# Kernel optimization log

Measured on AMD Instinct MI355X. Metric: run time of the kernel, lower is better.

## Reference

```python
import jax, jax.numpy as jnp
import numpy as np

B, T, IDIM = 16, 1024, 345
L, D, H, DK, FF = 4, 256, 4, 64, 1024
EPS = 1e-5


def layer_norm(x, s, b):
    m = jnp.mean(x, axis=-1, keepdims=True)
    v = jnp.mean(jnp.square(x - m), axis=-1, keepdims=True)
    return (x - m) * jax.lax.rsqrt(v + EPS) * s + b


def setup_inputs() -> dict:
    key = jax.random.key(0)
    ks = jax.random.split(key, 16)
    w = 0.02
    return {
        "x": jax.random.normal(ks[0], (B, T, IDIM), jnp.float32),
        "num_frames": int(T),
        "Win": w * jax.random.normal(ks[1], (IDIM, D), jnp.float32),
        "b_in": jnp.zeros((D,), jnp.float32),
        "ln1_s": jnp.ones((L, D), jnp.float32),
        "ln1_b": jnp.zeros((L, D), jnp.float32),
        "Wq": w * jax.random.normal(ks[2], (L, D, D), jnp.float32),
        "bq": jnp.zeros((L, D), jnp.float32),
        "Wk": w * jax.random.normal(ks[3], (L, D, D), jnp.float32),
        "bk": jnp.zeros((L, D), jnp.float32),
        "Wv": w * jax.random.normal(ks[4], (L, D, D), jnp.float32),
        "bv": jnp.zeros((L, D), jnp.float32),
        "Wo": w * jax.random.normal(ks[5], (L, D, D), jnp.float32),
        "bo": jnp.zeros((L, D), jnp.float32),
        "ln2_s": jnp.ones((L, D), jnp.float32),
        "ln2_b": jnp.zeros((L, D), jnp.float32),
        "W1": w * jax.random.normal(ks[6], (L, D, FF), jnp.float32),
        "b1": jnp.zeros((L, FF), jnp.float32),
        "W2": w * jax.random.normal(ks[7], (L, FF, D), jnp.float32),
        "b2": jnp.zeros((L, D), jnp.float32),
        "lno_s": jnp.ones((D,), jnp.float32),
        "lno_b": jnp.zeros((D,), jnp.float32),
    }


def reference(x, num_frames, Win, b_in, ln1_s, ln1_b, Wq, bq, Wk, bk, Wv, bv,
              Wo, bo, ln2_s, ln2_b, W1, b1, W2, b2, lno_s, lno_b):
    num = x.shape[0]
    scale = 1.0 / np.sqrt(DK)
    # [num*T, D]
    e = x.reshape(-1, x.shape[-1]) @ Win + b_in
    for i in range(L):
        e = layer_norm(e, ln1_s[i], ln1_b[i])
        # naive MHSA (residual taken from LN output, as in the source)
        q = (e @ Wq[i] + bq[i]).reshape(num, -1, H, DK)
        k = (e @ Wk[i] + bk[i]).reshape(num, -1, H, DK)
        v = (e @ Wv[i] + bv[i]).reshape(num, -1, H, DK)
        scores = jnp.einsum('bqhd,bkhd->bhqk', q, k) * scale
        attn = jax.nn.softmax(scores, axis=-1)
        o = jnp.einsum('bhqk,bkhd->bqhd', attn, v).reshape(-1, D)
        e = e + (o @ Wo[i] + bo[i])
        e = layer_norm(e, ln2_s[i], ln2_b[i])
        e = e + (jax.nn.relu(e @ W1[i] + b1[i]) @ W2[i] + b2[i])
    out = layer_norm(e, lno_s, lno_b)
    return out.reshape(num, num_frames, -1)
```

## Files before the change

kernel.cpp:

```cpp
#include <hip/hip_runtime.h>
#include <hip/hip_bf16.h>

#define BB    16
#define TT    1024
#define MTOK  (BB*TT)
#define IDIM_ 345
#define KPAD  384
#define LL    4
#define DD_   256
#define FF_   1024
#define EPS_  1e-5f
#define QSCL  0.18033688f
#define MSHIFT 12.0f

typedef __bf16 bf16;
typedef bf16 bf16x8 __attribute__((ext_vector_type(8)));
typedef float f32x4 __attribute__((ext_vector_type(4)));

static __device__ __forceinline__ f32x4 MFMA(bf16x8 a, bf16x8 b, f32x4 c) {
  return __builtin_amdgcn_mfma_f32_16x16x32_bf16(a, b, c, 0, 0, 0);
}
static __device__ __forceinline__ unsigned bfbits(float x) {
  return (unsigned)__builtin_bit_cast(unsigned short, (bf16)x);
}
static __device__ __forceinline__ bf16x8 ld_bf8(const void* p) {
  return *reinterpret_cast<const bf16x8*>(p);
}
static __device__ __forceinline__ void gload_lds16(const bf16* g, void* l) {
  __builtin_amdgcn_global_load_lds(
      (const __attribute__((address_space(1))) void*)g,
      (__attribute__((address_space(3))) void*)l, 16, 0, 0);
}

__global__ void k_convert_pad(const float* __restrict__ src, bf16* __restrict__ dst) {
  int idx = blockIdx.x * 256 + threadIdx.x;
  if (idx >= MTOK * (KPAD / 4)) return;
  int r = idx / (KPAD / 4), c0 = (idx % (KPAD / 4)) * 4;
  const float* s = src + (long)r * IDIM_ + c0;
  float v0 = (c0 + 0 < IDIM_) ? s[0] : 0.f;
  float v1 = (c0 + 1 < IDIM_) ? s[1] : 0.f;
  float v2 = (c0 + 2 < IDIM_) ? s[2] : 0.f;
  float v3 = (c0 + 3 < IDIM_) ? s[3] : 0.f;
  uint2 pk;
  pk.x = bfbits(v0) | (bfbits(v1) << 16);
  pk.y = bfbits(v2) | (bfbits(v3) << 16);
  *reinterpret_cast<uint2*>(dst + (long)r * KPAD + c0) = pk;
}

__global__ void k_wt_convert(const float* __restrict__ src, bf16* __restrict__ dst,
                             int K, int N, int Kp) {
  int idx = blockIdx.x * 256 + threadIdx.x;
  if (idx >= N * Kp) return;
  int n = idx / Kp, kk = idx % Kp;
  dst[idx] = (kk < K) ? (bf16)src[(long)kk * N + n] : (bf16)0.f;
}

__global__ __launch_bounds__(256)
void k_wt_all(const float* __restrict__ Wq, const float* __restrict__ Wk,
              const float* __restrict__ Wv, const float* __restrict__ Wo,
              const float* __restrict__ W1, const float* __restrict__ W2,
              bf16* __restrict__ Wqkvt, bf16* __restrict__ Wot,
              bf16* __restrict__ W1t, bf16* __restrict__ W2t) {
  __shared__ float tile[64][65];
  const int s = blockIdx.y, m = s >> 2, i = s & 3;
  const float* src; bf16* dst; int K, N;
  switch (m) {
    case 0: src = Wq + (long)i*65536;  dst = Wqkvt + (long)i*196608;          K=256;  N=256;  break;
    case 1: src = Wk + (long)i*65536;  dst = Wqkvt + (long)i*196608 + 65536;  K=256;  N=256;  break;
    case 2: src = Wv + (long)i*65536;  dst = Wqkvt + (long)i*196608 + 131072; K=256;  N=256;  break;
    case 3: src = Wo + (long)i*65536;  dst = Wot + (long)i*65536;             K=256;  N=256;  break;
    case 4: src = W1 + (long)i*262144; dst = W1t + (long)i*262144;            K=256;  N=1024; break;
    default:src = W2 + (long)i*262144; dst = W2t + (long)i*262144;            K=1024; N=256;  break;
  }
  const int tiles_n = N >> 6, ntiles = (K >> 6) * tiles_n;
  if (blockIdx.x >= ntiles) return;
  const int tk = blockIdx.x / tiles_n, tn = blockIdx.x % tiles_n;
  const int t = threadIdx.x, rq = t >> 6, cl = t & 63;
  #pragma unroll
  for (int i2 = 0; i2 < 16; i2++)
    tile[rq * 16 + i2][cl] = src[(long)(tk * 64 + rq * 16 + i2) * N + tn * 64 + cl];
  __syncthreads();
  #pragma unroll
  for (int i2 = 0; i2 < 16; i2++)
    dst[(long)(tn * 64 + rq * 16 + i2) * K + tk * 64 + cl] = (bf16)tile[cl][rq * 16 + i2];
}

__global__ void k_bias_concat(const float* __restrict__ bq, const float* __restrict__ bk,
                              const float* __restrict__ bv, float* __restrict__ bqkv) {
  int idx = blockIdx.x * 256 + threadIdx.x;
  if (idx >= LL * 768) return;
  int i = idx / 768, j = idx % 768;
  float v = (j < 256) ? bq[i*256 + j] : (j < 512 ? bk[i*256 + j - 256] : bv[i*256 + j - 512]);
  bqkv[idx] = v;
}

template<int EPI>
__global__ __launch_bounds__(512, 4)
void k_gemm_row(const bf16* __restrict__ A, const bf16* __restrict__ Wt,
                const float* __restrict__ bias, const bf16* __restrict__ resid,
                const float* __restrict__ lns, const float* __restrict__ lnb,
                void* __restrict__ out, int K) {
  __shared__ alignas(16) char As[4096];
  __shared__ alignas(16) char Bs[32768];
  __shared__ alignas(16) float redS[32][4];
  __shared__ alignas(16) float redQ[32][4];
  const int t = threadIdx.x, lane = t & 63, wid = t >> 6;
  const int wr = wid >> 2, wc = wid & 3;
  const int g = lane >> 4, c = lane & 15;
  int flat = blockIdx.x;
  flat = (flat & 7) * 64 + (flat >> 3);
  const int mbase = flat * 32;

  const int srow = t >> 3;
  const int slot = ((t & 7) ^ (srow & 7)) * 8;
  const bf16* ag = A  + (long)(mbase + srow) * K + slot;
  const bf16* bg = Wt + (long)srow * K + slot;
  const int swz = (c & 7) << 4;

  f32x4 acc[4] = {};

  const int nk = K >> 6;
  for (int kt = 0; kt < nk; ++kt) {
    const int k0 = kt * 64;
    __syncthreads();
    if (wid < 4) gload_lds16(ag + k0, As + wid * 1024);
    #pragma unroll
    for (int p = 0; p < 4; p++)
      gload_lds16(bg + (long)(p * 64) * K + k0, Bs + p * 8192 + wid * 1024);
    __syncthreads();

    bf16x8 af[2], bfr[4][2];
    #pragma unroll
    for (int ks = 0; ks < 2; ks++)
      af[ks] = ld_bf8(As + (wr * 16 + c) * 128 + ((ks * 64 + g * 16) ^ swz));
    #pragma unroll
    for (int ni = 0; ni < 4; ni++)
      #pragma unroll
      for (int ks = 0; ks < 2; ks++)
        bfr[ni][ks] = ld_bf8(Bs + (wc * 64 + ni * 16 + c) * 128 + ((ks * 64 + g * 16) ^ swz));
    __builtin_amdgcn_s_setprio(1);
    #pragma unroll
    for (int ni = 0; ni < 4; ni++)
      #pragma unroll
      for (int ks = 0; ks < 2; ks++)
        acc[ni] = MFMA(af[ks], bfr[ni][ks], acc[ni]);
    __builtin_amdgcn_s_setprio(0);
  }

  float v[4][4];
  float sP[4] = {0.f, 0.f, 0.f, 0.f}, qP[4] = {0.f, 0.f, 0.f, 0.f};
  #pragma unroll
  for (int ni = 0; ni < 4; ni++) {
    const int col = wc * 64 + ni * 16 + c;
    const float bb = bias[col];
    #pragma unroll
    for (int j = 0; j < 4; j++) {
      const int row = mbase + wr * 16 + g * 4 + j;
      float r = resid ? (float)resid[(long)row * 256 + col] : 0.f;
      float x = acc[ni][j] + bb + r;
      v[ni][j] = x;
      sP[j] += x;
      qP[j] += x * x;
    }
  }
  #pragma unroll
  for (int j = 0; j < 4; j++) {
    #pragma unroll
    for (int off = 1; off < 16; off <<= 1) {
      sP[j] += __shfl_xor(sP[j], off);
      qP[j] += __shfl_xor(qP[j], off);
    }
  }
  if (c == 0) {
    #pragma unroll
    for (int j = 0; j < 4; j++) {
      const int rb = wr * 16 + g * 4 + j;
      redS[rb][wc] = sP[j];
      redQ[rb][wc] = qP[j];
    }
  }
  __syncthreads();

  #pragma unroll
  for (int j = 0; j < 4; j++) {
    const int rb = wr * 16 + g * 4 + j;
    const float4 s4 = *reinterpret_cast<const float4*>(redS[rb]);
    const float4 q4 = *reinterpret_cast<const float4*>(redQ[rb]);
    const float mean = (s4.x + s4.y + s4.z + s4.w) * (1.f / 256.f);
    const float var = (q4.x + q4.y + q4.z + q4.w) * (1.f / 256.f) - mean * mean;
    const float rstd = rsqrtf(var + EPS_);
    const long row = mbase + wr * 16 + g * 4 + j;
    #pragma unroll
    for (int ni = 0; ni < 4; ni++) {
      const int col = wc * 64 + ni * 16 + c;
      const float y = (v[ni][j] - mean) * rstd * lns[col] + lnb[col];
      if constexpr (EPI == 0) {
        ((bf16*)out)[row * 256 + col] = (bf16)y;
      } else {
        ((float*)out)[row * 256 + col] = y;
      }
    }
  }
}

template<int EPI>
__global__ __launch_bounds__(256)
void k_gemm_big(const bf16* __restrict__ A, const bf16* __restrict__ Wt,
                const float* __restrict__ bias, void* __restrict__ out,
                bf16* __restrict__ vt, int N, int K) {
  __shared__ alignas(16) char As[16384];
  __shared__ alignas(16) char Bs[16384];
  const int t = threadIdx.x, lane = t & 63, wid = t >> 6;
  const int wr = wid >> 1, wc = wid & 1;
  const int g = lane >> 4, c = lane & 15;
  int flat = blockIdx.y * gridDim.x + blockIdx.x;
  const int cpx = (gridDim.x * gridDim.y) >> 3;
  flat = (flat & 7) * cpx + (flat >> 3);
  const int mbase = (flat / gridDim.x) * 128, nbase = (flat % gridDim.x) * 128;

  const int srow = t >> 3;
  const int skc = ((t & 7) ^ (srow & 7)) * 8;
  const bf16* ag = A  + (long)(mbase + srow) * K + skc;
  const bf16* bg = Wt + (long)(nbase + srow) * K + skc;
  const int swz = (c & 7) << 4;

  f32x4 acc[4][4] = {};

  const int nk = K >> 6;
  for (int kt = 0; kt < nk; ++kt) {
    const int k0 = kt * 64;
    __syncthreads();
    #pragma unroll
    for (int p = 0; p < 4; p++) {
      gload_lds16(ag + (long)p * 32 * K + k0, As + p * 4096 + wid * 1024);
      gload_lds16(bg + (long)p * 32 * K + k0, Bs + p * 4096 + wid * 1024);
    }
    __syncthreads();

    bf16x8 af[4][2], bfr[4][2];
    #pragma unroll
    for (int mi = 0; mi < 4; mi++)
      #pragma unroll
      for (int ks = 0; ks < 2; ks++)
        af[mi][ks] = ld_bf8(As + (wr * 64 + mi * 16 + c) * 128 + ((ks * 64 + g * 16) ^ swz));
    #pragma unroll
    for (int ni = 0; ni < 4; ni++)
      #pragma unroll
      for (int ks = 0; ks < 2; ks++)
        bfr[ni][ks] = ld_bf8(Bs + (wc * 64 + ni * 16 + c) * 128 + ((ks * 64 + g * 16) ^ swz));
    __builtin_amdgcn_s_setprio(1);
    #pragma unroll
    for (int mi = 0; mi < 4; mi++)
      #pragma unroll
      for (int ni = 0; ni < 4; ni++)
        #pragma unroll
        for (int ks = 0; ks < 2; ks++)
          acc[mi][ni] = MFMA(af[mi][ks], bfr[ni][ks], acc[mi][ni]);
    __builtin_amdgcn_s_setprio(0);
  }

  #pragma unroll
  for (int mi = 0; mi < 4; mi++) {
    #pragma unroll
    for (int ni = 0; ni < 4; ni++) {
      const int colg = nbase + wc * 64 + ni * 16 + c;
      const float bv = bias ? bias[colg] : 0.f;
      if constexpr (EPI == 3) {
        if (nbase < 512) {
          const float qs = (nbase < 256) ? QSCL : 1.0f;
          #pragma unroll
          for (int j = 0; j < 4; j++) {
            const int rowg = mbase + wr * 64 + mi * 16 + g * 4 + j;
            ((bf16*)out)[(long)rowg * N + colg] = (bf16)((acc[mi][ni][j] + bv) * qs);
          }
        } else {
          const int dfull = colg - 512, hh = dfull >> 6, d = dfull & 63;
          const int rowg0 = mbase + wr * 64 + mi * 16 + g * 4;
          uint2 st;
          st.x = bfbits(acc[mi][ni][0] + bv) | (bfbits(acc[mi][ni][1] + bv) << 16);
          st.y = bfbits(acc[mi][ni][2] + bv) | (bfbits(acc[mi][ni][3] + bv) << 16);
          *reinterpret_cast<uint2*>(vt + (long)(((rowg0 >> 10) << 2) + hh) * 65536
                                       + d * 1024 + (rowg0 & 1023)) = st;
        }
      } else {
        #pragma unroll
        for (int j = 0; j < 4; j++) {
          const int rowg = mbase + wr * 64 + mi * 16 + g * 4 + j;
          ((bf16*)out)[(long)rowg * N + colg] = (bf16)fmaxf(acc[mi][ni][j] + bv, 0.f);
        }
      }
    }
  }
}

__global__ __launch_bounds__(256)
void k_attn(const bf16* __restrict__ qkv, const bf16* __restrict__ vtg,
            bf16* __restrict__ o) {
  __shared__ alignas(16) char Ks[2][8192];
  __shared__ alignas(16) char Vs[2][8192];
  __shared__ alignas(16) char Ps[16384];
  const int t = threadIdx.x, lane = t & 63, w = t >> 6;
  const int g = lane >> 4, c = lane & 15;
  int flat = blockIdx.y * 8 + blockIdx.x;
  flat = (flat & 7) * 64 + (flat >> 3);
  const int bh = flat >> 3, qt = flat & 7;
  const int b = bh >> 2, h = bh & 3;
  const long tokbase = (long)b * TT;
  const int qA = qt * 128 + w * 16 + c;
  const int qB = qA + 64;

  bf16x8 qf0A = ld_bf8(qkv + (tokbase + qA) * 768 + h * 64 + g * 8);
  bf16x8 qf1A = ld_bf8(qkv + (tokbase + qA) * 768 + h * 64 + 32 + g * 8);
  bf16x8 qf0B = ld_bf8(qkv + (tokbase + qB) * 768 + h * 64 + g * 8);
  bf16x8 qf1B = ld_bf8(qkv + (tokbase + qB) * 768 + h * 64 + 32 + g * 8);

  const int sr = t >> 3;
  const int slot = (t & 7) ^ (sr & 7);
  const int swz_c = (c & 7) << 4;
  const bf16* kbase = qkv + 256 + h * 64 + slot * 8;
  const bf16* vbase = vtg + (long)bh * 65536 + slot * 8;
  char* pwA = Ps + w * 4096 + c * 128;
  char* pwB = pwA + 2048;

#define KSTAGE(bi, jt) do { \
    gload_lds16(kbase + (tokbase + (jt) * 64 + sr) * 768,      Ks[bi] + w * 1024); \
    gload_lds16(kbase + (tokbase + (jt) * 64 + sr + 32) * 768, Ks[bi] + 4096 + w * 1024); \
    gload_lds16(vbase + (long)sr * 1024 + (jt) * 64,           Vs[bi] + w * 1024); \
    gload_lds16(vbase + (long)(sr + 32) * 1024 + (jt) * 64,    Vs[bi] + 4096 + w * 1024); \
  } while (0)

  f32x4 oaccA[4] = {}, oaccB[4] = {};
  float lA = 0.f, lB = 0.f;

  KSTAGE(0, 0);
  int cur = 0;
  for (int jt = 0; jt < 16; ++jt) {
    if (jt + 1 < 16) {
      KSTAGE(cur ^ 1, jt + 1);
      asm volatile("s_waitcnt vmcnt(4)" ::: "memory");
    } else {
      asm volatile("s_waitcnt vmcnt(0)" ::: "memory");
    }
    __builtin_amdgcn_s_barrier();

    f32x4 saccA[4] = {}, saccB[4] = {};
    __builtin_amdgcn_s_setprio(1);
    #pragma unroll
    for (int ni = 0; ni < 4; ni++) {
      const char* krow = Ks[cur] + (ni * 16 + c) * 128;
      bf16x8 kf0 = ld_bf8(krow + ((g * 16) ^ swz_c));
      bf16x8 kf1 = ld_bf8(krow + ((64 + g * 16) ^ swz_c));
      saccA[ni] = MFMA(kf0, qf0A, saccA[ni]);
      saccB[ni] = MFMA(kf0, qf0B, saccB[ni]);
      saccA[ni] = MFMA(kf1, qf1A, saccA[ni]);
      saccB[ni] = MFMA(kf1, qf1B, saccB[ni]);
    }
    __builtin_amdgcn_s_setprio(0);

    #pragma unroll
    for (int ni = 0; ni < 4; ni++) {
      float a0 = __builtin_amdgcn_exp2f(saccA[ni][0] - MSHIFT);
      float b0 = __builtin_amdgcn_exp2f(saccB[ni][0] - MSHIFT);
      float a1 = __builtin_amdgcn_exp2f(saccA[ni][1] - MSHIFT);
      float b1 = __builtin_amdgcn_exp2f(saccB[ni][1] - MSHIFT);
      float a2 = __builtin_amdgcn_exp2f(saccA[ni][2] - MSHIFT);
      float b2 = __builtin_amdgcn_exp2f(saccB[ni][2] - MSHIFT);
      float a3 = __builtin_amdgcn_exp2f(saccA[ni][3] - MSHIFT);
      float b3 = __builtin_amdgcn_exp2f(saccB[ni][3] - MSHIFT);
      lA += (a0 + a1) + (a2 + a3);
      lB += (b0 + b1) + (b2 + b3);
      uint2 qa, qb;
      qa.x = bfbits(a0) | (bfbits(a1) << 16);
      qa.y = bfbits(a2) | (bfbits(a3) << 16);
      qb.x = bfbits(b0) | (bfbits(b1) << 16);
      qb.y = bfbits(b2) | (bfbits(b3) << 16);
      *reinterpret_cast<uint2*>(pwA + ((ni * 32 + g * 8) ^ swz_c)) = qa;
      *reinterpret_cast<uint2*>(pwB + ((ni * 32 + g * 8) ^ swz_c)) = qb;
    }

    __builtin_amdgcn_s_setprio(1);
    #pragma unroll
    for (int kk = 0; kk < 2; kk++) {
      bf16x8 pfA = ld_bf8(pwA + ((kk * 64 + g * 16) ^ swz_c));
      bf16x8 pfB = ld_bf8(pwB + ((kk * 64 + g * 16) ^ swz_c));
      #pragma unroll
      for (int nd = 0; nd < 4; nd++) {
        bf16x8 vf = ld_bf8(Vs[cur] + (nd * 16 + c) * 128 + ((kk * 64 + g * 16) ^ swz_c));
        oaccA[nd] = MFMA(vf, pfA, oaccA[nd]);
        oaccB[nd] = MFMA(vf, pfB, oaccB[nd]);
      }
    }
    __builtin_amdgcn_s_setprio(0);
    __builtin_amdgcn_s_barrier();
    cur ^= 1;
  }
#undef KSTAGE

  lA += __shfl_xor(lA, 16);
  lB += __shfl_xor(lB, 16);
  lA += __shfl_xor(lA, 32);
  lB += __shfl_xor(lB, 32);

  const float invA = 1.f / lA, invB = 1.f / lB;
  bf16* orowA = o + (tokbase + qA) * 256 + h * 64 + g * 4;
  bf16* orowB = o + (tokbase + qB) * 256 + h * 64 + g * 4;
  #pragma unroll
  for (int nd = 0; nd < 4; nd++) {
    uint2 sa, sb;
    sa.x = bfbits(oaccA[nd][0] * invA) | (bfbits(oaccA[nd][1] * invA) << 16);
    sa.y = bfbits(oaccA[nd][2] * invA) | (bfbits(oaccA[nd][3] * invA) << 16);
    sb.x = bfbits(oaccB[nd][0] * invB) | (bfbits(oaccB[nd][1] * invB) << 16);
    sb.y = bfbits(oaccB[nd][2] * invB) | (bfbits(oaccB[nd][3] * invB) << 16);
    *reinterpret_cast<uint2*>(orowA + nd * 16) = sa;
    *reinterpret_cast<uint2*>(orowB + nd * 16) = sb;
  }
}

extern "C" void kernel_launch(void* const* d_in, const int* in_sizes, int n_in,
                              void* d_out, int out_size, void* d_ws, size_t ws_size,
                              hipStream_t stream) {
  const float* x     = (const float*)d_in[0];
  const float* Win   = (const float*)d_in[2];
  const float* b_in  = (const float*)d_in[3];
  const float* ln1_s = (const float*)d_in[4];
  const float* ln1_b = (const float*)d_in[5];
  const float* Wq    = (const float*)d_in[6];
  const float* bq    = (const float*)d_in[7];
  const float* Wk    = (const float*)d_in[8];
  const float* bk    = (const float*)d_in[9];
  const float* Wv    = (const float*)d_in[10];
  const float* bv    = (const float*)d_in[11];
  const float* Wo    = (const float*)d_in[12];
  const float* bo    = (const float*)d_in[13];
  const float* ln2_s = (const float*)d_in[14];
  const float* ln2_b = (const float*)d_in[15];
  const float* W1    = (const float*)d_in[16];
  const float* b1    = (const float*)d_in[17];
  const float* W2    = (const float*)d_in[18];
  const float* b2    = (const float*)d_in[19];
  const float* lno_s = (const float*)d_in[20];
  const float* lno_b = (const float*)d_in[21];
  float* out = (float*)d_out;

  char* ws = (char*)d_ws;
  size_t off = 0;
  auto alloc = [&](size_t bytes) -> void* {
    void* p = ws + off; off += (bytes + 255) & ~(size_t)255; return p;
  };
  bf16* e_bf  = (bf16*)alloc((size_t)MTOK * DD_ * 2);
  bf16* qkvb  = (bf16*)alloc((size_t)MTOK * 768 * 2);
  bf16* vtb   = (bf16*)alloc((size_t)MTOK * DD_ * 2);
  bf16* ob    = (bf16*)alloc((size_t)MTOK * DD_ * 2);
  bf16* hb    = (bf16*)alloc((size_t)MTOK * FF_ * 2);
  bf16* x_bf  = (bf16*)hb;
  bf16* Wint  = (bf16*)alloc((size_t)DD_ * KPAD * 2);
  bf16* Wqkvt = (bf16*)alloc((size_t)LL * 768 * DD_ * 2);
  bf16* Wot   = (bf16*)alloc((size_t)LL * DD_ * DD_ * 2);
  bf16* W1t   = (bf16*)alloc((size_t)LL * DD_ * FF_ * 2);
  bf16* W2t   = (bf16*)alloc((size_t)LL * FF_ * DD_ * 2);
  float* bqkv = (float*)alloc((size_t)LL * 768 * 4);

  dim3 blk(256);

  k_convert_pad<<<(MTOK * (KPAD / 4) + 255) / 256, 256, 0, stream>>>(x, x_bf);
  k_wt_convert<<<(DD_ * KPAD + 255) / 256, 256, 0, stream>>>(Win, Wint, IDIM_, DD_, KPAD);
  k_wt_all<<<dim3(64, 24), blk, 0, stream>>>(Wq, Wk, Wv, Wo, W1, W2, Wqkvt, Wot, W1t, W2t);
  k_bias_concat<<<(LL * 768 + 255) / 256, 256, 0, stream>>>(bq, bk, bv, bqkv);

  k_gemm_row<0><<<512, 512, 0, stream>>>(x_bf, Wint, b_in, nullptr,
                                         ln1_s, ln1_b, e_bf, KPAD);

  const long DDW = (long)DD_ * DD_;
  const long DFF = (long)DD_ * FF_;
  for (int i = 0; i < LL; i++) {
    k_gemm_big<3><<<dim3(6, 128), blk, 0, stream>>>(e_bf, Wqkvt + (long)i * 768 * DD_,
                                                    bqkv + i * 768, qkvb, vtb, 768, DD_);
    k_attn<<<dim3(8, 64), blk, 0, stream>>>(qkvb, vtb, ob);
    k_gemm_row<0><<<512, 512, 0, stream>>>(ob, Wot + i * DDW, bo + i * DD_, e_bf,
                                           ln2_s + i * DD_, ln2_b + i * DD_, e_bf, DD_);
    k_gemm_big<1><<<dim3(8, 128), blk, 0, stream>>>(e_bf, W1t + i * DFF, b1 + i * FF_,
                                                    hb, nullptr, FF_, DD_);
    if (i < LL - 1) {
      k_gemm_row<0><<<512, 512, 0, stream>>>(hb, W2t + i * DFF, b2 + i * DD_, e_bf,
                                             ln1_s + (i + 1) * DD_, ln1_b + (i + 1) * DD_,
                                             e_bf, FF_);
    } else {
      k_gemm_row<1><<<512, 512, 0, stream>>>(hb, W2t + i * DFF, b2 + i * DD_, e_bf,
                                             lno_s, lno_b, out, FF_);
    }
  }
}
```

Before: 424.9 us.

## Fuse FFN up-projection, ReLU, down-projection and LayerNorm into one kernel

Replaces the separate W1 GEMM (writing a 16K x 1024 bf16 hidden buffer) and the W2 row-GEMM with a single kernel. Each block keeps a 32-row activation tile in LDS and computes the hidden tile in 256-column chunks, applying ReLU into LDS. Each chunk is immediately consumed by the W2 accumulation, followed by the residual add and LayerNorm. This removes the global write and read of the hidden activations. In exchange, each block re-streams both full weight matrices with small 32-row tiles and more barriers, which raises weight traffic and may lower MFMA efficiency.

```diff
diff --git a/kernel.cpp b/kernel.cpp
--- a/kernel.cpp
+++ b/kernel.cpp
@@ -204,6 +204,164 @@
 }
 
 template<int EPI>
+__global__ __launch_bounds__(512, 4)
+void k_ffn(const bf16* __restrict__ e, const bf16* __restrict__ W1t,
+           const float* __restrict__ b1, const bf16* __restrict__ W2t,
+           const float* __restrict__ b2, const float* __restrict__ lns,
+           const float* __restrict__ lnb, void* __restrict__ out) {
+  __shared__ alignas(16) char Ae[16384];
+  __shared__ alignas(16) char Hs[16384];
+  __shared__ alignas(16) char Bs[32768];
+  __shared__ alignas(16) float redS[32][4];
+  __shared__ alignas(16) float redQ[32][4];
+  const int t = threadIdx.x, lane = t & 63, wid = t >> 6;
+  const int wr = wid >> 2, wc = wid & 3;
+  const int g = lane >> 4, c = lane & 15;
+  int flat = blockIdx.x;
+  flat = (flat & 7) * 64 + (flat >> 3);
+  const int mbase = flat * 32;
+  const int swz = (c & 7) << 4;
+
+  #pragma unroll
+  for (int p = 0; p < 2; p++) {
+    const int ch = p * 512 + t;
+    const int row = ch >> 5, s = ch & 31;
+    const int srcb = (s >> 3) * 128 + (((s & 7) ^ (row & 7)) << 4);
+    gload_lds16(e + (long)(mbase + row) * 256 + (srcb >> 1),
+                Ae + p * 8192 + wid * 1024);
+  }
+
+  const int srow = t >> 3;
+  const int slot = ((t & 7) ^ (srow & 7)) * 8;
+  const int arow = wr * 16 + c;
+  const int axo = (arow & 7) << 4;
+
+  f32x4 acc2[4] = {};
+  asm volatile("s_waitcnt vmcnt(0)" ::: "memory");
+  __builtin_amdgcn_s_barrier();
+
+  #pragma unroll 1
+  for (int q = 0; q < 4; q++) {
+    f32x4 acc1[4] = {};
+    const bf16* bg1 = W1t + (long)(q * 256 + srow) * 256 + slot;
+    for (int kt = 0; kt < 4; ++kt) {
+      __syncthreads();
+      #pragma unroll
+      for (int p = 0; p < 4; p++)
+        gload_lds16(bg1 + (long)(p * 64) * 256 + kt * 64, Bs + p * 8192 + wid * 1024);
+      __syncthreads();
+      bf16x8 af[2], bfr[4][2];
+      #pragma unroll
+      for (int ks = 0; ks < 2; ks++)
+        af[ks] = ld_bf8(Ae + arow * 512 + ((kt * 128 + ks * 64 + g * 16) ^ axo));
+      #pragma unroll
+      for (int ni = 0; ni < 4; ni++)
+        #pragma unroll
+        for (int ks = 0; ks < 2; ks++)
+          bfr[ni][ks] = ld_bf8(Bs + (wc * 64 + ni * 16 + c) * 128 + ((ks * 64 + g * 16) ^ swz));
+      __builtin_amdgcn_s_setprio(1);
+      #pragma unroll
+      for (int ni = 0; ni < 4; ni++)
+        #pragma unroll
+        for (int ks = 0; ks < 2; ks++)
+          acc1[ni] = MFMA(af[ks], bfr[ni][ks], acc1[ni]);
+      __builtin_amdgcn_s_setprio(0);
+    }
+    #pragma unroll
+    for (int ni = 0; ni < 4; ni++) {
+      const int col = wc * 64 + ni * 16 + c;
+      const float bb = b1[q * 256 + col];
+      #pragma unroll
+      for (int j = 0; j < 4; j++) {
+        const int row = wr * 16 + g * 4 + j;
+        *(bf16*)(Hs + row * 512 + ((col * 2) ^ ((row & 7) << 4))) =
+            (bf16)fmaxf(acc1[ni][j] + bb, 0.f);
+      }
+    }
+    __syncthreads();
+    const bf16* bg2 = W2t + (long)srow * 1024 + q * 256 + slot;
+    for (int kt = 0; kt < 4; ++kt) {
+      __syncthreads();
+      #pragma unroll
+      for (int p = 0; p < 4; p++)
+        gload_lds16(bg2 + (long)(p * 64) * 1024 + kt * 64, Bs + p * 8192 + wid * 1024);
+      __syncthreads();
+      bf16x8 af[2], bfr[4][2];
+      #pragma unroll
+      for (int ks = 0; ks < 2; ks++)
+        af[ks] = ld_bf8(Hs + arow * 512 + ((kt * 128 + ks * 64 + g * 16) ^ axo));
+      #pragma unroll
+      for (int ni = 0; ni < 4; ni++)
+        #pragma unroll
+        for (int ks = 0; ks < 2; ks++)
+          bfr[ni][ks] = ld_bf8(Bs + (wc * 64 + ni * 16 + c) * 128 + ((ks * 64 + g * 16) ^ swz));
+      __builtin_amdgcn_s_setprio(1);
+      #pragma unroll
+      for (int ni = 0; ni < 4; ni++)
+        #pragma unroll
+        for (int ks = 0; ks < 2; ks++)
+          acc2[ni] = MFMA(af[ks], bfr[ni][ks], acc2[ni]);
+      __builtin_amdgcn_s_setprio(0);
+    }
+  }
+
+  float v[4][4];
+  float sP[4] = {0.f, 0.f, 0.f, 0.f}, qP[4] = {0.f, 0.f, 0.f, 0.f};
+  #pragma unroll
+  for (int ni = 0; ni < 4; ni++) {
+    const int col = wc * 64 + ni * 16 + c;
+    const float bb = b2[col];
+    #pragma unroll
+    for (int j = 0; j < 4; j++) {
+      const int row = wr * 16 + g * 4 + j;
+      float r = (float)*(const bf16*)(Ae + row * 512 + ((col * 2) ^ ((row & 7) << 4)));
+      float x = acc2[ni][j] + bb + r;
+      v[ni][j] = x;
+      sP[j] += x;
+      qP[j] += x * x;
+    }
+  }
+  #pragma unroll
+  for (int j = 0; j < 4; j++) {
+    #pragma unroll
+    for (int off = 1; off < 16; off <<= 1) {
+      sP[j] += __shfl_xor(sP[j], off);
+      qP[j] += __shfl_xor(qP[j], off);
+    }
+  }
+  if (c == 0) {
+    #pragma unroll
+    for (int j = 0; j < 4; j++) {
+      const int rb = wr * 16 + g * 4 + j;
+      redS[rb][wc] = sP[j];
+      redQ[rb][wc] = qP[j];
+    }
+  }
+  __syncthreads();
+
+  #pragma unroll
+  for (int j = 0; j < 4; j++) {
+    const int rb = wr * 16 + g * 4 + j;
+    const float4 s4 = *reinterpret_cast<const float4*>(redS[rb]);
+    const float4 q4 = *reinterpret_cast<const float4*>(redQ[rb]);
+    const float mean = (s4.x + s4.y + s4.z + s4.w) * (1.f / 256.f);
+    const float var = (q4.x + q4.y + q4.z + q4.w) * (1.f / 256.f) - mean * mean;
+    const float rstd = rsqrtf(var + EPS_);
+    const long row = mbase + wr * 16 + g * 4 + j;
+    #pragma unroll
+    for (int ni = 0; ni < 4; ni++) {
+      const int col = wc * 64 + ni * 16 + c;
+      const float y = (v[ni][j] - mean) * rstd * lns[col] + lnb[col];
+      if constexpr (EPI == 0) {
+        ((bf16*)out)[row * 256 + col] = (bf16)y;
+      } else {
+        ((float*)out)[row * 256 + col] = y;
+      }
+    }
+  }
+}
+
+template<int EPI>
 __global__ __launch_bounds__(256)
 void k_gemm_big(const bf16* __restrict__ A, const bf16* __restrict__ Wt,
                 const float* __restrict__ bias, void* __restrict__ out,
@@ -265,29 +423,21 @@
     for (int ni = 0; ni < 4; ni++) {
       const int colg = nbase + wc * 64 + ni * 16 + c;
       const float bv = bias ? bias[colg] : 0.f;
-      if constexpr (EPI == 3) {
-        if (nbase < 512) {
-          const float qs = (nbase < 256) ? QSCL : 1.0f;
-          #pragma unroll
-          for (int j = 0; j < 4; j++) {
-            const int rowg = mbase + wr * 64 + mi * 16 + g * 4 + j;
-            ((bf16*)out)[(long)rowg * N + colg] = (bf16)((acc[mi][ni][j] + bv) * qs);
-          }
-        } else {
-          const int dfull = colg - 512, hh = dfull >> 6, d = dfull & 63;
-          const int rowg0 = mbase + wr * 64 + mi * 16 + g * 4;
-          uint2 st;
-          st.x = bfbits(acc[mi][ni][0] + bv) | (bfbits(acc[mi][ni][1] + bv) << 16);
-          st.y = bfbits(acc[mi][ni][2] + bv) | (bfbits(acc[mi][ni][3] + bv) << 16);
-          *reinterpret_cast<uint2*>(vt + (long)(((rowg0 >> 10) << 2) + hh) * 65536
-                                       + d * 1024 + (rowg0 & 1023)) = st;
-        }
-      } else {
+      if (nbase < 512) {
+        const float qs = (nbase < 256) ? QSCL : 1.0f;
         #pragma unroll
         for (int j = 0; j < 4; j++) {
           const int rowg = mbase + wr * 64 + mi * 16 + g * 4 + j;
-          ((bf16*)out)[(long)rowg * N + colg] = (bf16)fmaxf(acc[mi][ni][j] + bv, 0.f);
+          ((bf16*)out)[(long)rowg * N + colg] = (bf16)((acc[mi][ni][j] + bv) * qs);
         }
+      } else {
+        const int dfull = colg - 512, hh = dfull >> 6, d = dfull & 63;
+        const int rowg0 = mbase + wr * 64 + mi * 16 + g * 4;
+        uint2 st;
+        st.x = bfbits(acc[mi][ni][0] + bv) | (bfbits(acc[mi][ni][1] + bv) << 16);
+        st.y = bfbits(acc[mi][ni][2] + bv) | (bfbits(acc[mi][ni][3] + bv) << 16);
+        *reinterpret_cast<uint2*>(vt + (long)(((rowg0 >> 10) << 2) + hh) * 65536
+                                     + d * 1024 + (rowg0 & 1023)) = st;
       }
     }
   }
@@ -451,8 +601,7 @@
   bf16* qkvb  = (bf16*)alloc((size_t)MTOK * 768 * 2);
   bf16* vtb   = (bf16*)alloc((size_t)MTOK * DD_ * 2);
   bf16* ob    = (bf16*)alloc((size_t)MTOK * DD_ * 2);
-  bf16* hb    = (bf16*)alloc((size_t)MTOK * FF_ * 2);
-  bf16* x_bf  = (bf16*)hb;
+  bf16* x_bf  = (bf16*)alloc((size_t)MTOK * KPAD * 2);
   bf16* Wint  = (bf16*)alloc((size_t)DD_ * KPAD * 2);
   bf16* Wqkvt = (bf16*)alloc((size_t)LL * 768 * DD_ * 2);
   bf16* Wot   = (bf16*)alloc((size_t)LL * DD_ * DD_ * 2);
@@ -478,15 +627,14 @@
     k_attn<<<dim3(8, 64), blk, 0, stream>>>(qkvb, vtb, ob);
     k_gemm_row<0><<<512, 512, 0, stream>>>(ob, Wot + i * DDW, bo + i * DD_, e_bf,
                                            ln2_s + i * DD_, ln2_b + i * DD_, e_bf, DD_);
-    k_gemm_big<1><<<dim3(8, 128), blk, 0, stream>>>(e_bf, W1t + i * DFF, b1 + i * FF_,
-                                                    hb, nullptr, FF_, DD_);
     if (i < LL - 1) {
-      k_gemm_row<0><<<512, 512, 0, stream>>>(hb, W2t + i * DFF, b2 + i * DD_, e_bf,
-                                             ln1_s + (i + 1) * DD_, ln1_b + (i + 1) * DD_,
-                                             e_bf, FF_);
+      k_ffn<0><<<512, 512, 0, stream>>>(e_bf, W1t + i * DFF, b1 + i * FF_,
+                                        W2t + i * DFF, b2 + i * DD_,
+                                        ln1_s + (i + 1) * DD_, ln1_b + (i + 1) * DD_, e_bf);
     } else {
-      k_gemm_row<1><<<512, 512, 0, stream>>>(hb, W2t + i * DFF, b2 + i * DD_, e_bf,
-                                             lno_s, lno_b, out, FF_);
-    }
-  }
-}
+      k_ffn<1><<<512, 512, 0, stream>>>(e_bf, W1t + i * DFF, b1 + i * FF_,
+                                        W2t + i * DFF, b2 + i * DD_,
+                                        lno_s, lno_b, out);
+    }
+  }
+}
```

Result: faster. 410.8 us, median of 3 (-3.3%).
